# Performance work log

Measured on AMD Instinct MI355X. Metric: run time of the kernel, lower is better.

## Reference

```python
import jax, jax.numpy as jnp
import numpy as np

B, D = 8192, 2048
H1, H2, G = 1024, 512, 512
T, SPEC, SH = 2, 2, 2
E = T * SPEC + SH          # total experts = 6
EC = SPEC + SH             # experts per task = 4


def setup_inputs() -> dict:
    key = jax.random.key(0)
    ks = jax.random.split(key, 6)
    s = 0.02  # glorot-ish scale
    return {
        "x":   jax.random.normal(ks[0], (B, D), jnp.float32),
        "We1": jax.random.normal(ks[1], (E, D, H1), jnp.float32) * s,
        "be1": jnp.zeros((E, H1), jnp.float32),
        "We2": jax.random.normal(ks[2], (E, H1, H2), jnp.float32) * s,
        "be2": jnp.zeros((E, H2), jnp.float32),
        "Wg1": jax.random.normal(ks[3], (T, D, G), jnp.float32) * s,
        "bg1": jnp.zeros((T, G), jnp.float32),
        "Wgs": jax.random.normal(ks[4], (T, G, EC), jnp.float32) * s,
    }


# per-task expert indices: task i uses its SPEC specific experts + the SH shared (last) experts
_IDX = np.array([[i * SPEC + j for j in range(SPEC)] + list(range(T * SPEC, E))
                 for i in range(T)])  # [T, EC]


def reference(x, We1, be1, We2, be2, Wg1, bg1, Wgs):
    # All experts batched into grouped GEMMs (the fusion the original loop misses)
    h1 = jax.nn.relu(jnp.einsum('bd,edh->beh', x, We1) + be1)        # [B,E,H1]
    h2 = jax.nn.relu(jnp.einsum('beh,eho->beo', h1, We2) + be2)      # [B,E,H2]
    # Gate MLP per task, batched over tasks
    g = jax.nn.relu(jnp.einsum('bd,tdg->btg', x, Wg1) + bg1)         # [B,T,G]
    gate = jax.nn.softmax(jnp.einsum('btg,tge->bte', g, Wgs), axis=-1)  # [B,T,EC]
    sel = h2[:, _IDX, :]                                             # [B,T,EC,H2]
    out = jnp.einsum('bteo,bte->tbo', sel, gate)                     # [T,B,H2]
    return out
```

## Files before the change

kernel.cpp:

```cpp
#include <hip/hip_runtime.h>
#include <hip/hip_bf16.h>
#include <cstdint>
#include <cstddef>

#define B_   8192
#define D_   2048
#define H1_  1024
#define H2_  512
#define G_   512
#define T_   2
#define E_   6
#define EC_  4

typedef __bf16 bf16_t;
typedef __attribute__((ext_vector_type(8))) __bf16 bf16x8;
typedef __attribute__((ext_vector_type(4))) float f32x4;

__device__ __forceinline__ void gload_lds16(const bf16_t* g, bf16_t* l) {
    __builtin_amdgcn_global_load_lds(
        (const __attribute__((address_space(1))) bf16_t*)g,
        (__attribute__((address_space(3))) bf16_t*)l,
        16, 0, 0);
}

__global__ __launch_bounds__(256) void cast_x_kernel(
    const float* __restrict__ src, bf16_t* __restrict__ dst, int n8)
{
    int i = blockIdx.x * blockDim.x + threadIdx.x;
    if (i >= n8) return;
    const float4* s = (const float4*)src + (size_t)i * 2;
    float4 a = s[0], b = s[1];
    bf16x8 o;
    o[0] = (bf16_t)a.x; o[1] = (bf16_t)a.y; o[2] = (bf16_t)a.z; o[3] = (bf16_t)a.w;
    o[4] = (bf16_t)b.x; o[5] = (bf16_t)b.y; o[6] = (bf16_t)b.z; o[7] = (bf16_t)b.w;
    *(bf16x8*)(dst + (size_t)i * 8) = o;
}

__global__ __launch_bounds__(256) void transpose_cast_kernel(
    const float* __restrict__ src, bf16_t* __restrict__ dst, int R, int C)
{
    __shared__ float tile[32][33];
    int bz = blockIdx.z;
    src += (size_t)bz * R * C;
    dst += (size_t)bz * R * C;
    int c0 = blockIdx.x * 32, r0 = blockIdx.y * 32;
    int tx = threadIdx.x, ty = threadIdx.y;
#pragma unroll
    for (int i = 0; i < 32; i += 8)
        tile[ty + i][tx] = src[(size_t)(r0 + ty + i) * C + (c0 + tx)];
    __syncthreads();
#pragma unroll
    for (int i = 0; i < 32; i += 8)
        dst[(size_t)(c0 + ty + i) * R + (r0 + tx)] = (bf16_t)tile[tx][ty + i];
}

__global__ __launch_bounds__(512, 2) void gemm256_8p1b(
    const bf16_t* __restrict__ A, const bf16_t* __restrict__ Bt,
    const float* __restrict__ bias, bf16_t* __restrict__ C,
    int M, int N, int K, long long strideA)
{
    const int e = blockIdx.z;
    A    += (size_t)e * (size_t)strideA;
    Bt   += (size_t)e * (size_t)N * (size_t)K;
    bias += (size_t)e * (size_t)N;
    C    += (size_t)e * (size_t)M * (size_t)N;

    const int gx  = gridDim.x;
    const int nwg = gx * gridDim.y;
    const int lin = blockIdx.y * gx + blockIdx.x;
    const int swz = (lin & 7) * (nwg >> 3) + (lin >> 3);
    const int bx  = swz % gx;
    const int by  = swz / gx;
    const int row0 = by * 256;
    const int col0 = bx * 256;

    __shared__ bf16_t lsA[2][16384];
    __shared__ bf16_t lsB[2][16384];

    const int tid  = threadIdx.x;
    const int lane = tid & 63;
    const int wave = tid >> 6;
    const int wr   = wave >> 2;
    const int wc   = wave & 3;

    size_t offG[2];
    int    ldsOff[2];
#pragma unroll
    for (int l = 0; l < 2; ++l) {
        int idx = l * 512 + tid;
        int r   = idx >> 3;
        int c   = (idx & 7) ^ (r & 7);
        offG[l]   = (size_t)r * (size_t)K + (size_t)(c * 8);
        ldsOff[l] = l * 4096 + wave * 512;
    }
    const bf16_t* gA = A  + (size_t)row0 * (size_t)K;
    const bf16_t* gB = Bt + (size_t)col0 * (size_t)K;
    const size_t halfStride = (size_t)128 * (size_t)K;

    const int rbA = (wr * 128 + (lane & 15)) * 64;
    const int rbB = (wc * 64  + (lane & 15)) * 64;
    int xc[2];
#pragma unroll
    for (int ks = 0; ks < 2; ++ks)
        xc[ks] = (ks * 32 + ((lane >> 4) * 8)) ^ ((lane & 7) << 3);

    f32x4 acc[8][4];
#pragma unroll
    for (int m = 0; m < 8; ++m)
#pragma unroll
        for (int n = 0; n < 4; ++n)
            acc[m][n] = (f32x4){0.f, 0.f, 0.f, 0.f};

    const int nt    = K >> 6;
    const int niter = nt >> 1;

#define STAGE_A(dst, kt, h) do {                                              \
    _Pragma("unroll")                                                         \
    for (int l_ = 0; l_ < 2; ++l_)                                            \
        gload_lds16(gA + (size_t)((kt) * 64) + (size_t)(h) * halfStride       \
                       + offG[l_],                                            \
                    &lsA[dst][(h) * 8192 + ldsOff[l_]]);                      \
} while (0)

#define STAGE_B(dst, kt, h) do {                                              \
    _Pragma("unroll")                                                         \
    for (int l_ = 0; l_ < 2; ++l_)                                            \
        gload_lds16(gB + (size_t)((kt) * 64) + (size_t)(h) * halfStride       \
                       + offG[l_],                                            \
                    &lsB[dst][(h) * 8192 + ldsOff[l_]]);                      \
} while (0)

#define PHASE(d, qm, STMT, WAITV) do {                                        \
    bf16x8 af00, af01, af10, af11;                                            \
    af00 = *(const bf16x8*)&lsA[d][rbA + (2*(qm)+0) * 1024 + xc[0]];          \
    af01 = *(const bf16x8*)&lsA[d][rbA + (2*(qm)+0) * 1024 + xc[1]];          \
    af10 = *(const bf16x8*)&lsA[d][rbA + (2*(qm)+1) * 1024 + xc[0]];          \
    af11 = *(const bf16x8*)&lsA[d][rbA + (2*(qm)+1) * 1024 + xc[1]];          \
    if ((qm) == 0) {                                                          \
        _Pragma("unroll")                                                     \
        for (int n_ = 0; n_ < 4; ++n_) {                                      \
            bfr[n_][0] = *(const bf16x8*)&lsB[d][rbB + n_ * 1024 + xc[0]];    \
            bfr[n_][1] = *(const bf16x8*)&lsB[d][rbB + n_ * 1024 + xc[1]];    \
        }                                                                     \
    }                                                                         \
    STMT;                                                                     \
    WAITV;                                                                    \
    __builtin_amdgcn_sched_barrier(0);                                        \
    __builtin_amdgcn_s_barrier();                                             \
    asm volatile("s_waitcnt lgkmcnt(0)" ::: "memory");                        \
    __builtin_amdgcn_sched_barrier(0);                                        \
    __builtin_amdgcn_s_setprio(1);                                            \
    _Pragma("unroll")                                                         \
    for (int n_ = 0; n_ < 4; ++n_) {                                          \
        acc[2*(qm)+0][n_] = __builtin_amdgcn_mfma_f32_16x16x32_bf16(          \
                                af00, bfr[n_][0], acc[2*(qm)+0][n_], 0,0,0);  \
        acc[2*(qm)+0][n_] = __builtin_amdgcn_mfma_f32_16x16x32_bf16(          \
                                af01, bfr[n_][1], acc[2*(qm)+0][n_], 0,0,0);  \
        acc[2*(qm)+1][n_] = __builtin_amdgcn_mfma_f32_16x16x32_bf16(          \
                                af10, bfr[n_][0], acc[2*(qm)+1][n_], 0,0,0);  \
        acc[2*(qm)+1][n_] = __builtin_amdgcn_mfma_f32_16x16x32_bf16(          \
                                af11, bfr[n_][1], acc[2*(qm)+1][n_], 0,0,0);  \
    }                                                                         \
    __builtin_amdgcn_s_setprio(0);                                            \
    __builtin_amdgcn_sched_barrier(0);                                        \
} while (0)

    STAGE_A(0, 0, 0); STAGE_A(0, 0, 1);
    STAGE_B(0, 0, 0); STAGE_B(0, 0, 1);
    STAGE_B(1, 1, 0); STAGE_B(1, 1, 1);
    asm volatile("s_waitcnt vmcnt(4)" ::: "memory");
    __builtin_amdgcn_sched_barrier(0);
    __builtin_amdgcn_s_barrier();
    __builtin_amdgcn_sched_barrier(0);

    for (int i = 0; i < niter; ++i) {
        const int kt0 = 2 * i, kt1 = 2 * i + 1;
        const bool stg = (i + 1 < niter);
        bf16x8 bfr[4][2];

        PHASE(0, 0, { STAGE_A(1, kt1, 0); }, {});
        PHASE(0, 1, { STAGE_A(1, kt1, 1); }, {});
        PHASE(0, 2, { if (stg) STAGE_B(0, kt0 + 2, 0); }, {});
        PHASE(0, 3, { if (stg) STAGE_B(0, kt0 + 2, 1); },
              { if (stg) { asm volatile("s_waitcnt vmcnt(4)" ::: "memory"); }
                else     { asm volatile("s_waitcnt vmcnt(0)" ::: "memory"); } });
        PHASE(1, 0, { if (stg) STAGE_A(0, kt0 + 2, 0); }, {});
        PHASE(1, 1, { if (stg) STAGE_A(0, kt0 + 2, 1); }, {});
        PHASE(1, 2, { if (stg) STAGE_B(1, kt0 + 3, 0); }, {});
        PHASE(1, 3, { if (stg) STAGE_B(1, kt0 + 3, 1); },
              { if (stg) { asm volatile("s_waitcnt vmcnt(4)" ::: "memory"); } });
    }
#undef PHASE
#undef STAGE_A
#undef STAGE_B

    const int crb = row0 + wr * 128 + ((lane >> 4) << 2);
    const int ccb = col0 + wc * 64  + (lane & 15);
#pragma unroll
    for (int n = 0; n < 4; ++n) {
        const int cc = ccb + n * 16;
        const float bv = bias[cc];
#pragma unroll
        for (int m = 0; m < 8; ++m) {
            const int rb = crb + m * 16;
#pragma unroll
            for (int j = 0; j < 4; ++j) {
                float v = acc[m][n][j] + bv;
                v = v > 0.f ? v : 0.f;
                C[(size_t)(rb + j) * N + cc] = (bf16_t)v;
            }
        }
    }
}

__global__ __launch_bounds__(512, 4) void gemm_bn256_bias_relu(
    const bf16_t* __restrict__ A, const bf16_t* __restrict__ Bt,
    const float* __restrict__ bias, bf16_t* __restrict__ C,
    int M, int N, int K, long long strideA)
{
    const int e = blockIdx.z;
    A    += (size_t)e * (size_t)strideA;
    Bt   += (size_t)e * (size_t)N * (size_t)K;
    bias += (size_t)e * (size_t)N;
    C    += (size_t)e * (size_t)M * (size_t)N;

    const int gx  = gridDim.x;
    const int nwg = gx * gridDim.y;
    const int lin = blockIdx.y * gx + blockIdx.x;
    const int swz = (lin & 7) * (nwg >> 3) + (lin >> 3);
    const int row0 = (swz / gx) * 128;
    const int col0 = (swz % gx) * 256;

    __shared__ bf16_t lsA[3][128 * 32];
    __shared__ bf16_t lsB[3][256 * 32];

    const int tid  = threadIdx.x;
    const int lane = tid & 63;
    const int wave = tid >> 6;
    const int wr   = wave >> 2;
    const int wc   = wave & 3;

    size_t offA, offB0, offB1;
    {
        int rA = tid >> 2, pA = tid & 3;
        offA = (size_t)rA * (size_t)K + (size_t)(((pA ^ (rA >> 1)) & 3) * 8);
        int r0_ = tid >> 2, p0_ = tid & 3;
        offB0 = (size_t)r0_ * (size_t)K + (size_t)(((p0_ ^ (r0_ >> 1)) & 3) * 8);
        int r1_ = (512 + tid) >> 2, p1_ = tid & 3;
        offB1 = (size_t)r1_ * (size_t)K + (size_t)(((p1_ ^ (r1_ >> 1)) & 3) * 8);
    }
    const int ldsA_off = wave * 512;
    const int ldsB0off = wave * 512;
    const int ldsB1off = 4096 + wave * 512;

    const bf16_t* gA = A  + (size_t)row0 * (size_t)K;
    const bf16_t* gB = Bt + (size_t)col0 * (size_t)K;

    const int xch  = ((lane >> 4) ^ ((lane >> 1) & 3)) << 3;
    const int aoff = (wr * 64 + (lane & 15)) * 32 + xch;
    const int boff = (wc * 64 + (lane & 15)) * 32 + xch;

    f32x4 acc[4][4];
#pragma unroll
    for (int m = 0; m < 4; ++m)
#pragma unroll
        for (int n = 0; n < 4; ++n)
            acc[m][n] = (f32x4){0.f, 0.f, 0.f, 0.f};

    const int nt = K >> 5;

#define STAGE(t_, c_) do {                                                    \
    const size_t kk_ = (size_t)(t_) * 32;                                     \
    gload_lds16(gA + kk_ + offA,  &lsA[c_][ldsA_off]);                        \
    gload_lds16(gB + kk_ + offB0, &lsB[c_][ldsB0off]);                        \
    gload_lds16(gB + kk_ + offB1, &lsB[c_][ldsB1off]);                        \
} while (0)

    STAGE(0, 0); STAGE(1, 1); STAGE(2, 2);
    asm volatile("s_waitcnt vmcnt(6)" ::: "memory");
    __builtin_amdgcn_s_barrier();
    __builtin_amdgcn_sched_barrier(0);

    int c = 0;
    for (int t = 0; t < nt; ++t) {
        bf16x8 a[4], b[4];
#pragma unroll
        for (int m = 0; m < 4; ++m)
            a[m] = *(const bf16x8*)&lsA[c][aoff + m * 512];
#pragma unroll
        for (int n = 0; n < 4; ++n)
            b[n] = *(const bf16x8*)&lsB[c][boff + n * 512];
        asm volatile("s_waitcnt lgkmcnt(0)" ::: "memory");
        __builtin_amdgcn_sched_barrier(0);
        __builtin_amdgcn_s_barrier();
        __builtin_amdgcn_sched_barrier(0);
        if (t + 3 < nt) STAGE(t + 3, c);
        __builtin_amdgcn_sched_barrier(0);
        __builtin_amdgcn_s_setprio(1);
#pragma unroll
        for (int m = 0; m < 4; ++m)
#pragma unroll
            for (int n = 0; n < 4; ++n)
                acc[m][n] = __builtin_amdgcn_mfma_f32_16x16x32_bf16(
                                a[m], b[n], acc[m][n], 0, 0, 0);
        __builtin_amdgcn_s_setprio(0);
        __builtin_amdgcn_sched_barrier(0);
        if (t + 3 < nt) { asm volatile("s_waitcnt vmcnt(6)" ::: "memory"); }
        else            { asm volatile("s_waitcnt vmcnt(0)" ::: "memory"); }
        __builtin_amdgcn_sched_barrier(0);
        __builtin_amdgcn_s_barrier();
        __builtin_amdgcn_sched_barrier(0);
        c = (c == 2) ? 0 : c + 1;
    }
#undef STAGE

    const int crb = row0 + wr * 64 + ((lane >> 4) << 2);
    const int ccb = col0 + wc * 64 + (lane & 15);
#pragma unroll
    for (int n = 0; n < 4; ++n) {
        const int cc = ccb + n * 16;
        const float bv = bias[cc];
#pragma unroll
        for (int m = 0; m < 4; ++m) {
            const int rb = crb + m * 16;
#pragma unroll
            for (int j = 0; j < 4; ++j) {
                float v = acc[m][n][j] + bv;
                v = v > 0.f ? v : 0.f;
                C[(size_t)(rb + j) * N + cc] = (bf16_t)v;
            }
        }
    }
}

__global__ __launch_bounds__(256) void gate_kernel(
    const bf16_t* __restrict__ h1, const float* __restrict__ Wgs,
    float* __restrict__ gate)
{
    int wid  = blockIdx.x * 4 + (threadIdx.x >> 6);
    int lane = threadIdx.x & 63;
    int t = wid >> 13;
    int b = wid & (B_ - 1);
    const bf16_t* grow = h1 + ((size_t)(6 * B_) + b) * 1024 + t * G_;
    bf16x8 gv = *(const bf16x8*)&grow[lane * 8];
    const float* W = Wgs + (size_t)t * G_ * EC_;
    float a0 = 0.f, a1 = 0.f, a2 = 0.f, a3 = 0.f;
#pragma unroll
    for (int i = 0; i < 8; ++i) {
        float gvf = (float)gv[i];
        const float4 w = *(const float4*)&W[(size_t)(lane * 8 + i) * 4];
        a0 += gvf * w.x; a1 += gvf * w.y; a2 += gvf * w.z; a3 += gvf * w.w;
    }
#pragma unroll
    for (int off = 32; off; off >>= 1) {
        a0 += __shfl_xor(a0, off);
        a1 += __shfl_xor(a1, off);
        a2 += __shfl_xor(a2, off);
        a3 += __shfl_xor(a3, off);
    }
    if (lane == 0) {
        float m  = fmaxf(fmaxf(a0, a1), fmaxf(a2, a3));
        float e0 = expf(a0 - m), e1 = expf(a1 - m), e2 = expf(a2 - m), e3 = expf(a3 - m);
        float inv = 1.f / (e0 + e1 + e2 + e3);
        *(float4*)&gate[(size_t)wid * 4] = make_float4(e0 * inv, e1 * inv, e2 * inv, e3 * inv);
    }
}

__global__ __launch_bounds__(256) void combine_kernel(
    const bf16_t* __restrict__ h2, const float* __restrict__ gate,
    float* __restrict__ out)
{
    size_t idx = (size_t)blockIdx.x * 256 + threadIdx.x;
    size_t tb  = idx >> 6;
    int    o0  = (int)(idx & 63) * 8;
    int    t   = (int)(tb >> 13);
    size_t b   = tb & (size_t)(B_ - 1);
    const float4 gv = *(const float4*)&gate[tb * 4];
    const bf16x8 v0 = *(const bf16x8*)&h2[((size_t)(2 * t)     * B_ + b) * H2_ + o0];
    const bf16x8 v1 = *(const bf16x8*)&h2[((size_t)(2 * t + 1) * B_ + b) * H2_ + o0];
    const bf16x8 v2 = *(const bf16x8*)&h2[((size_t)4           * B_ + b) * H2_ + o0];
    const bf16x8 v3 = *(const bf16x8*)&h2[((size_t)5           * B_ + b) * H2_ + o0];
    float r[8];
#pragma unroll
    for (int i = 0; i < 8; ++i)
        r[i] = gv.x * (float)v0[i] + gv.y * (float)v1[i]
             + gv.z * (float)v2[i] + gv.w * (float)v3[i];
    float4* op = (float4*)&out[tb * H2_ + o0];
    op[0] = make_float4(r[0], r[1], r[2], r[3]);
    op[1] = make_float4(r[4], r[5], r[6], r[7]);
}

extern "C" void kernel_launch(void* const* d_in, const int* in_sizes, int n_in,
                              void* d_out, int out_size, void* d_ws, size_t ws_size,
                              hipStream_t stream)
{
    const float* x   = (const float*)d_in[0];
    const float* We1 = (const float*)d_in[1];
    const float* be1 = (const float*)d_in[2];
    const float* We2 = (const float*)d_in[3];
    const float* be2 = (const float*)d_in[4];
    const float* Wg1 = (const float*)d_in[5];
    const float* bg1 = (const float*)d_in[6];
    const float* Wgs = (const float*)d_in[7];
    float* out = (float*)d_out;

    char* ws = (char*)d_ws;
    bf16_t* x_bf  = (bf16_t*)ws;  ws += (size_t)B_ * D_ * 2;
    bf16_t* w1t   = (bf16_t*)ws;  ws += (size_t)7 * H1_ * D_ * 2;
    bf16_t* w2t   = (bf16_t*)ws;  ws += (size_t)E_ * H2_ * H1_ * 2;
    bf16_t* h1    = (bf16_t*)ws;  ws += (size_t)7 * B_ * H1_ * 2;
    bf16_t* h2    = (bf16_t*)ws;  ws += (size_t)E_ * B_ * H2_ * 2;
    float*  bias7 = (float*)ws;   ws += (size_t)7 * H1_ * 4;
    float*  gate  = (float*)ws;   ws += (size_t)T_ * B_ * EC_ * 4;

    bf16_t* wgt = w1t + (size_t)6 * H1_ * D_;

    hipMemcpyAsync(bias7, be1, (size_t)E_ * H1_ * sizeof(float),
                   hipMemcpyDeviceToDevice, stream);
    hipMemcpyAsync(bias7 + (size_t)E_ * H1_, bg1, (size_t)T_ * G_ * sizeof(float),
                   hipMemcpyDeviceToDevice, stream);

    cast_x_kernel<<<(B_ * D_ / 8) / 256, 256, 0, stream>>>(x, x_bf, B_ * D_ / 8);
    dim3 tb(32, 8);
    transpose_cast_kernel<<<dim3(H1_ / 32, D_ / 32, E_),  tb, 0, stream>>>(We1, w1t, D_,  H1_);
    transpose_cast_kernel<<<dim3(H2_ / 32, H1_ / 32, E_), tb, 0, stream>>>(We2, w2t, H1_, H2_);
    transpose_cast_kernel<<<dim3(G_ / 32, D_ / 32, T_),   tb, 0, stream>>>(Wg1, wgt, D_,  G_);

    gemm256_8p1b<<<dim3(H1_ / 256, B_ / 256, 7), 512, 0, stream>>>(
        x_bf, w1t, bias7, h1, B_, H1_, D_, 0LL);
    gemm_bn256_bias_relu<<<dim3(H2_ / 256, B_ / 128, E_), 512, 0, stream>>>(
        h1, w2t, be2, h2, B_, H2_, H1_, (long long)B_ * H1_);

    gate_kernel<<<(T_ * B_) / 4, 256, 0, stream>>>(h1, Wgs, gate);
    combine_kernel<<<((size_t)T_ * B_ * H2_ / 8) / 256, 256, 0, stream>>>(h2, gate, out);
}
```

Before: 383.8 us.

## Fuse gated combine into second GEMM epilogue with atomics; merge prep kernels

The second expert GEMM now scales its ReLU output by the per-row gate weights and atomically adds into the output. This removes the h2 intermediate buffer and the separate combine kernel, with the output zeroed by a memset beforehand. The x cast and the three weight transpose-casts are merged into one launch, and the first-layer bias now comes straight from be1/bg1, so the two device-to-device copies are gone. In exchange the epilogue issues scattered fp32 atomic adds (two per element for shared experts), and the summation order is no longer deterministic.

```diff
diff --git a/kernel.cpp b/kernel.cpp
--- a/kernel.cpp
+++ b/kernel.cpp
@@ -23,28 +23,42 @@
         16, 0, 0);
 }
 
-__global__ __launch_bounds__(256) void cast_x_kernel(
-    const float* __restrict__ src, bf16_t* __restrict__ dst, int n8)
-{
-    int i = blockIdx.x * blockDim.x + threadIdx.x;
-    if (i >= n8) return;
-    const float4* s = (const float4*)src + (size_t)i * 2;
-    float4 a = s[0], b = s[1];
-    bf16x8 o;
-    o[0] = (bf16_t)a.x; o[1] = (bf16_t)a.y; o[2] = (bf16_t)a.z; o[3] = (bf16_t)a.w;
-    o[4] = (bf16_t)b.x; o[5] = (bf16_t)b.y; o[6] = (bf16_t)b.z; o[7] = (bf16_t)b.w;
-    *(bf16x8*)(dst + (size_t)i * 8) = o;
-}
-
-__global__ __launch_bounds__(256) void transpose_cast_kernel(
-    const float* __restrict__ src, bf16_t* __restrict__ dst, int R, int C)
+__global__ __launch_bounds__(256) void prep_kernel(
+    const float* __restrict__ x,   const float* __restrict__ We1,
+    const float* __restrict__ We2, const float* __restrict__ Wg1,
+    bf16_t* __restrict__ x_bf, bf16_t* __restrict__ w1t,
+    bf16_t* __restrict__ w2t,  bf16_t* __restrict__ wgt)
 {
     __shared__ float tile[32][33];
-    int bz = blockIdx.z;
-    src += (size_t)bz * R * C;
-    dst += (size_t)bz * R * C;
-    int c0 = blockIdx.x * 32, r0 = blockIdx.y * 32;
-    int tx = threadIdx.x, ty = threadIdx.y;
+    const int z  = blockIdx.z;
+    const int bx = blockIdx.x, by = blockIdx.y;
+    const int tx = threadIdx.x, ty = threadIdx.y;
+
+    const float* src; bf16_t* dst; int R, C;
+    if (z < 6) {
+        src = We1 + (size_t)z * D_ * H1_;  dst = w1t + (size_t)z * H1_ * D_;
+        R = D_;  C = H1_;
+    } else if (z < 12) {
+        if (bx >= 16 || by >= 32) return;
+        src = We2 + (size_t)(z - 6) * H1_ * H2_;
+        dst = w2t + (size_t)(z - 6) * H2_ * H1_;
+        R = H1_; C = H2_;
+    } else if (z < 14) {
+        if (bx >= 16) return;
+        src = Wg1 + (size_t)(z - 12) * D_ * G_;
+        dst = wgt + (size_t)(z - 12) * G_ * D_;
+        R = D_;  C = G_;
+    } else {
+        int i = ((z - 14) * 2048 + by * 32 + bx) * 256 + ty * 32 + tx;
+        const float4* s = (const float4*)x + (size_t)i * 2;
+        float4 a = s[0], b = s[1];
+        bf16x8 o;
+        o[0] = (bf16_t)a.x; o[1] = (bf16_t)a.y; o[2] = (bf16_t)a.z; o[3] = (bf16_t)a.w;
+        o[4] = (bf16_t)b.x; o[5] = (bf16_t)b.y; o[6] = (bf16_t)b.z; o[7] = (bf16_t)b.w;
+        *(bf16x8*)(x_bf + (size_t)i * 8) = o;
+        return;
+    }
+    const int c0 = bx * 32, r0 = by * 32;
 #pragma unroll
     for (int i = 0; i < 32; i += 8)
         tile[ty + i][tx] = src[(size_t)(r0 + ty + i) * C + (c0 + tx)];
@@ -56,23 +70,21 @@
 
 __global__ __launch_bounds__(512, 2) void gemm256_8p1b(
     const bf16_t* __restrict__ A, const bf16_t* __restrict__ Bt,
-    const float* __restrict__ bias, bf16_t* __restrict__ C,
-    int M, int N, int K, long long strideA)
+    const float* __restrict__ be1, const float* __restrict__ bg1,
+    bf16_t* __restrict__ C, int M, int N, int K, long long strideA)
 {
     const int e = blockIdx.z;
-    A    += (size_t)e * (size_t)strideA;
-    Bt   += (size_t)e * (size_t)N * (size_t)K;
-    bias += (size_t)e * (size_t)N;
-    C    += (size_t)e * (size_t)M * (size_t)N;
+    A  += (size_t)e * (size_t)strideA;
+    Bt += (size_t)e * (size_t)N * (size_t)K;
+    C  += (size_t)e * (size_t)M * (size_t)N;
+    const float* bias = (e < 6) ? (be1 + (size_t)e * H1_) : bg1;
 
     const int gx  = gridDim.x;
     const int nwg = gx * gridDim.y;
     const int lin = blockIdx.y * gx + blockIdx.x;
     const int swz = (lin & 7) * (nwg >> 3) + (lin >> 3);
-    const int bx  = swz % gx;
-    const int by  = swz / gx;
-    const int row0 = by * 256;
-    const int col0 = bx * 256;
+    const int row0 = (swz / gx) * 256;
+    const int col0 = (swz % gx) * 256;
 
     __shared__ bf16_t lsA[2][16384];
     __shared__ bf16_t lsB[2][16384];
@@ -213,126 +225,6 @@
     }
 }
 
-__global__ __launch_bounds__(512, 4) void gemm_bn256_bias_relu(
-    const bf16_t* __restrict__ A, const bf16_t* __restrict__ Bt,
-    const float* __restrict__ bias, bf16_t* __restrict__ C,
-    int M, int N, int K, long long strideA)
-{
-    const int e = blockIdx.z;
-    A    += (size_t)e * (size_t)strideA;
-    Bt   += (size_t)e * (size_t)N * (size_t)K;
-    bias += (size_t)e * (size_t)N;
-    C    += (size_t)e * (size_t)M * (size_t)N;
-
-    const int gx  = gridDim.x;
-    const int nwg = gx * gridDim.y;
-    const int lin = blockIdx.y * gx + blockIdx.x;
-    const int swz = (lin & 7) * (nwg >> 3) + (lin >> 3);
-    const int row0 = (swz / gx) * 128;
-    const int col0 = (swz % gx) * 256;
-
-    __shared__ bf16_t lsA[3][128 * 32];
-    __shared__ bf16_t lsB[3][256 * 32];
-
-    const int tid  = threadIdx.x;
-    const int lane = tid & 63;
-    const int wave = tid >> 6;
-    const int wr   = wave >> 2;
-    const int wc   = wave & 3;
-
-    size_t offA, offB0, offB1;
-    {
-        int rA = tid >> 2, pA = tid & 3;
-        offA = (size_t)rA * (size_t)K + (size_t)(((pA ^ (rA >> 1)) & 3) * 8);
-        int r0_ = tid >> 2, p0_ = tid & 3;
-        offB0 = (size_t)r0_ * (size_t)K + (size_t)(((p0_ ^ (r0_ >> 1)) & 3) * 8);
-        int r1_ = (512 + tid) >> 2, p1_ = tid & 3;
-        offB1 = (size_t)r1_ * (size_t)K + (size_t)(((p1_ ^ (r1_ >> 1)) & 3) * 8);
-    }
-    const int ldsA_off = wave * 512;
-    const int ldsB0off = wave * 512;
-    const int ldsB1off = 4096 + wave * 512;
-
-    const bf16_t* gA = A  + (size_t)row0 * (size_t)K;
-    const bf16_t* gB = Bt + (size_t)col0 * (size_t)K;
-
-    const int xch  = ((lane >> 4) ^ ((lane >> 1) & 3)) << 3;
-    const int aoff = (wr * 64 + (lane & 15)) * 32 + xch;
-    const int boff = (wc * 64 + (lane & 15)) * 32 + xch;
-
-    f32x4 acc[4][4];
-#pragma unroll
-    for (int m = 0; m < 4; ++m)
-#pragma unroll
-        for (int n = 0; n < 4; ++n)
-            acc[m][n] = (f32x4){0.f, 0.f, 0.f, 0.f};
-
-    const int nt = K >> 5;
-
-#define STAGE(t_, c_) do {                                                    \
-    const size_t kk_ = (size_t)(t_) * 32;                                     \
-    gload_lds16(gA + kk_ + offA,  &lsA[c_][ldsA_off]);                        \
-    gload_lds16(gB + kk_ + offB0, &lsB[c_][ldsB0off]);                        \
-    gload_lds16(gB + kk_ + offB1, &lsB[c_][ldsB1off]);                        \
-} while (0)
-
-    STAGE(0, 0); STAGE(1, 1); STAGE(2, 2);
-    asm volatile("s_waitcnt vmcnt(6)" ::: "memory");
-    __builtin_amdgcn_s_barrier();
-    __builtin_amdgcn_sched_barrier(0);
-
-    int c = 0;
-    for (int t = 0; t < nt; ++t) {
-        bf16x8 a[4], b[4];
-#pragma unroll
-        for (int m = 0; m < 4; ++m)
-            a[m] = *(const bf16x8*)&lsA[c][aoff + m * 512];
-#pragma unroll
-        for (int n = 0; n < 4; ++n)
-            b[n] = *(const bf16x8*)&lsB[c][boff + n * 512];
-        asm volatile("s_waitcnt lgkmcnt(0)" ::: "memory");
-        __builtin_amdgcn_sched_barrier(0);
-        __builtin_amdgcn_s_barrier();
-        __builtin_amdgcn_sched_barrier(0);
-        if (t + 3 < nt) STAGE(t + 3, c);
-        __builtin_amdgcn_sched_barrier(0);
-        __builtin_amdgcn_s_setprio(1);
-#pragma unroll
-        for (int m = 0; m < 4; ++m)
-#pragma unroll
-            for (int n = 0; n < 4; ++n)
-                acc[m][n] = __builtin_amdgcn_mfma_f32_16x16x32_bf16(
-                                a[m], b[n], acc[m][n], 0, 0, 0);
-        __builtin_amdgcn_s_setprio(0);
-        __builtin_amdgcn_sched_barrier(0);
-        if (t + 3 < nt) { asm volatile("s_waitcnt vmcnt(6)" ::: "memory"); }
-        else            { asm volatile("s_waitcnt vmcnt(0)" ::: "memory"); }
-        __builtin_amdgcn_sched_barrier(0);
-        __builtin_amdgcn_s_barrier();
-        __builtin_amdgcn_sched_barrier(0);
-        c = (c == 2) ? 0 : c + 1;
-    }
-#undef STAGE
-
-    const int crb = row0 + wr * 64 + ((lane >> 4) << 2);
-    const int ccb = col0 + wc * 64 + (lane & 15);
-#pragma unroll
-    for (int n = 0; n < 4; ++n) {
-        const int cc = ccb + n * 16;
-        const float bv = bias[cc];
-#pragma unroll
-        for (int m = 0; m < 4; ++m) {
-            const int rb = crb + m * 16;
-#pragma unroll
-            for (int j = 0; j < 4; ++j) {
-                float v = acc[m][n][j] + bv;
-                v = v > 0.f ? v : 0.f;
-                C[(size_t)(rb + j) * N + cc] = (bf16_t)v;
-            }
-        }
-    }
-}
-
 __global__ __launch_bounds__(256) void gate_kernel(
     const bf16_t* __restrict__ h1, const float* __restrict__ Wgs,
     float* __restrict__ gate)
@@ -366,28 +258,138 @@
     }
 }
 
-__global__ __launch_bounds__(256) void combine_kernel(
-    const bf16_t* __restrict__ h2, const float* __restrict__ gate,
-    float* __restrict__ out)
+__global__ __launch_bounds__(512, 4) void gemm2_gated(
+    const bf16_t* __restrict__ A, const bf16_t* __restrict__ Bt,
+    const float* __restrict__ bias, const float* __restrict__ gate,
+    float* __restrict__ out, int M, int N, int K, long long strideA)
 {
-    size_t idx = (size_t)blockIdx.x * 256 + threadIdx.x;
-    size_t tb  = idx >> 6;
-    int    o0  = (int)(idx & 63) * 8;
-    int    t   = (int)(tb >> 13);
-    size_t b   = tb & (size_t)(B_ - 1);
-    const float4 gv = *(const float4*)&gate[tb * 4];
-    const bf16x8 v0 = *(const bf16x8*)&h2[((size_t)(2 * t)     * B_ + b) * H2_ + o0];
-    const bf16x8 v1 = *(const bf16x8*)&h2[((size_t)(2 * t + 1) * B_ + b) * H2_ + o0];
-    const bf16x8 v2 = *(const bf16x8*)&h2[((size_t)4           * B_ + b) * H2_ + o0];
-    const bf16x8 v3 = *(const bf16x8*)&h2[((size_t)5           * B_ + b) * H2_ + o0];
-    float r[8];
-#pragma unroll
-    for (int i = 0; i < 8; ++i)
-        r[i] = gv.x * (float)v0[i] + gv.y * (float)v1[i]
-             + gv.z * (float)v2[i] + gv.w * (float)v3[i];
-    float4* op = (float4*)&out[tb * H2_ + o0];
-    op[0] = make_float4(r[0], r[1], r[2], r[3]);
-    op[1] = make_float4(r[4], r[5], r[6], r[7]);
+    const int e = blockIdx.z;
+    A    += (size_t)e * (size_t)strideA;
+    Bt   += (size_t)e * (size_t)N * (size_t)K;
+    bias += (size_t)e * (size_t)N;
+
+    const int gx  = gridDim.x;
+    const int nwg = gx * gridDim.y;
+    const int lin = blockIdx.y * gx + blockIdx.x;
+    const int swz = (lin & 7) * (nwg >> 3) + (lin >> 3);
+    const int row0 = (swz / gx) * 128;
+    const int col0 = (swz % gx) * 256;
+
+    __shared__ bf16_t lsA[3][128 * 32];
+    __shared__ bf16_t lsB[3][256 * 32];
+
+    const int tid  = threadIdx.x;
+    const int lane = tid & 63;
+    const int wave = tid >> 6;
+    const int wr   = wave >> 2;
+    const int wc   = wave & 3;
+
+    size_t offA, offB0, offB1;
+    {
+        int rA = tid >> 2, pA = tid & 3;
+        offA = (size_t)rA * (size_t)K + (size_t)(((pA ^ (rA >> 1)) & 3) * 8);
+        int r0_ = tid >> 2, p0_ = tid & 3;
+        offB0 = (size_t)r0_ * (size_t)K + (size_t)(((p0_ ^ (r0_ >> 1)) & 3) * 8);
+        int r1_ = (512 + tid) >> 2, p1_ = tid & 3;
+        offB1 = (size_t)r1_ * (size_t)K + (size_t)(((p1_ ^ (r1_ >> 1)) & 3) * 8);
+    }
+    const int ldsA_off = wave * 512;
+    const int ldsB0off = wave * 512;
+    const int ldsB1off = 4096 + wave * 512;
+
+    const bf16_t* gA = A  + (size_t)row0 * (size_t)K;
+    const bf16_t* gB = Bt + (size_t)col0 * (size_t)K;
+
+    const int xch  = ((lane >> 4) ^ ((lane >> 1) & 3)) << 3;
+    const int aoff = (wr * 64 + (lane & 15)) * 32 + xch;
+    const int boff = (wc * 64 + (lane & 15)) * 32 + xch;
+
+    f32x4 acc[4][4];
+#pragma unroll
+    for (int m = 0; m < 4; ++m)
+#pragma unroll
+        for (int n = 0; n < 4; ++n)
+            acc[m][n] = (f32x4){0.f, 0.f, 0.f, 0.f};
+
+    const int nt = K >> 5;
+
+#define STAGE(t_, c_) do {                                                    \
+    const size_t kk_ = (size_t)(t_) * 32;                                     \
+    gload_lds16(gA + kk_ + offA,  &lsA[c_][ldsA_off]);                        \
+    gload_lds16(gB + kk_ + offB0, &lsB[c_][ldsB0off]);                        \
+    gload_lds16(gB + kk_ + offB1, &lsB[c_][ldsB1off]);                        \
+} while (0)
+
+    STAGE(0, 0); STAGE(1, 1); STAGE(2, 2);
+    asm volatile("s_waitcnt vmcnt(6)" ::: "memory");
+    __builtin_amdgcn_s_barrier();
+    __builtin_amdgcn_sched_barrier(0);
+
+    int c = 0;
+    for (int t = 0; t < nt; ++t) {
+        bf16x8 a[4], b[4];
+#pragma unroll
+        for (int m = 0; m < 4; ++m)
+            a[m] = *(const bf16x8*)&lsA[c][aoff + m * 512];
+#pragma unroll
+        for (int n = 0; n < 4; ++n)
+            b[n] = *(const bf16x8*)&lsB[c][boff + n * 512];
+        asm volatile("s_waitcnt lgkmcnt(0)" ::: "memory");
+        __builtin_amdgcn_sched_barrier(0);
+        __builtin_amdgcn_s_barrier();
+        __builtin_amdgcn_sched_barrier(0);
+        if (t + 3 < nt) STAGE(t + 3, c);
+        __builtin_amdgcn_sched_barrier(0);
+        __builtin_amdgcn_s_setprio(1);
+#pragma unroll
+        for (int m = 0; m < 4; ++m)
+#pragma unroll
+            for (int n = 0; n < 4; ++n)
+                acc[m][n] = __builtin_amdgcn_mfma_f32_16x16x32_bf16(
+                                a[m], b[n], acc[m][n], 0, 0, 0);
+        __builtin_amdgcn_s_setprio(0);
+        __builtin_amdgcn_sched_barrier(0);
+        if (t + 3 < nt) { asm volatile("s_waitcnt vmcnt(6)" ::: "memory"); }
+        else            { asm volatile("s_waitcnt vmcnt(0)" ::: "memory"); }
+        __builtin_amdgcn_sched_barrier(0);
+        __builtin_amdgcn_s_barrier();
+        __builtin_amdgcn_sched_barrier(0);
+        c = (c == 2) ? 0 : c + 1;
+    }
+#undef STAGE
+
+    int t0, j0, t1 = -1, j1 = 0;
+    switch (e) {
+        case 0:  t0 = 0; j0 = 0; break;
+        case 1:  t0 = 0; j0 = 1; break;
+        case 2:  t0 = 1; j0 = 0; break;
+        case 3:  t0 = 1; j0 = 1; break;
+        case 4:  t0 = 0; j0 = 2; t1 = 1; j1 = 2; break;
+        default: t0 = 0; j0 = 3; t1 = 1; j1 = 3; break;
+    }
+    const int crb = row0 + wr * 64 + ((lane >> 4) << 2);
+    const int ccb = col0 + wc * 64 + (lane & 15);
+#pragma unroll
+    for (int n = 0; n < 4; ++n) {
+        const int cc = ccb + n * 16;
+        const float bv = bias[cc];
+#pragma unroll
+        for (int m = 0; m < 4; ++m) {
+            const int rb = crb + m * 16;
+#pragma unroll
+            for (int j = 0; j < 4; ++j) {
+                const int b = rb + j;
+                float v = acc[m][n][j] + bv;
+                v = v > 0.f ? v : 0.f;
+                float g0 = gate[((size_t)t0 * B_ + b) * EC_ + j0];
+                unsafeAtomicAdd(&out[((size_t)t0 * B_ + b) * H2_ + cc], g0 * v);
+                if (t1 >= 0) {
+                    float g1 = gate[((size_t)t1 * B_ + b) * EC_ + j1];
+                    unsafeAtomicAdd(&out[((size_t)t1 * B_ + b) * H2_ + cc], g1 * v);
+                }
+            }
+        }
+    }
 }
 
 extern "C" void kernel_launch(void* const* d_in, const int* in_sizes, int n_in,
@@ -405,32 +407,24 @@
     float* out = (float*)d_out;
 
     char* ws = (char*)d_ws;
-    bf16_t* x_bf  = (bf16_t*)ws;  ws += (size_t)B_ * D_ * 2;
-    bf16_t* w1t   = (bf16_t*)ws;  ws += (size_t)7 * H1_ * D_ * 2;
-    bf16_t* w2t   = (bf16_t*)ws;  ws += (size_t)E_ * H2_ * H1_ * 2;
-    bf16_t* h1    = (bf16_t*)ws;  ws += (size_t)7 * B_ * H1_ * 2;
-    bf16_t* h2    = (bf16_t*)ws;  ws += (size_t)E_ * B_ * H2_ * 2;
-    float*  bias7 = (float*)ws;   ws += (size_t)7 * H1_ * 4;
-    float*  gate  = (float*)ws;   ws += (size_t)T_ * B_ * EC_ * 4;
+    bf16_t* x_bf = (bf16_t*)ws;  ws += (size_t)B_ * D_ * 2;
+    bf16_t* w1t  = (bf16_t*)ws;  ws += (size_t)7 * H1_ * D_ * 2;
+    bf16_t* w2t  = (bf16_t*)ws;  ws += (size_t)E_ * H2_ * H1_ * 2;
+    bf16_t* h1   = (bf16_t*)ws;  ws += (size_t)7 * B_ * H1_ * 2;
+    float*  gate = (float*)ws;   ws += (size_t)T_ * B_ * EC_ * 4;
 
     bf16_t* wgt = w1t + (size_t)6 * H1_ * D_;
 
-    hipMemcpyAsync(bias7, be1, (size_t)E_ * H1_ * sizeof(float),
-                   hipMemcpyDeviceToDevice, stream);
-    hipMemcpyAsync(bias7 + (size_t)E_ * H1_, bg1, (size_t)T_ * G_ * sizeof(float),
-                   hipMemcpyDeviceToDevice, stream);
-
-    cast_x_kernel<<<(B_ * D_ / 8) / 256, 256, 0, stream>>>(x, x_bf, B_ * D_ / 8);
-    dim3 tb(32, 8);
-    transpose_cast_kernel<<<dim3(H1_ / 32, D_ / 32, E_),  tb, 0, stream>>>(We1, w1t, D_,  H1_);
-    transpose_cast_kernel<<<dim3(H2_ / 32, H1_ / 32, E_), tb, 0, stream>>>(We2, w2t, H1_, H2_);
-    transpose_cast_kernel<<<dim3(G_ / 32, D_ / 32, T_),   tb, 0, stream>>>(Wg1, wgt, D_,  G_);
+    hipMemsetAsync(out, 0, (size_t)T_ * B_ * H2_ * sizeof(float), stream);
+
+    prep_kernel<<<dim3(32, 64, 18), dim3(32, 8), 0, stream>>>(
+        x, We1, We2, Wg1, x_bf, w1t, w2t, wgt);
 
     gemm256_8p1b<<<dim3(H1_ / 256, B_ / 256, 7), 512, 0, stream>>>(
-        x_bf, w1t, bias7, h1, B_, H1_, D_, 0LL);
-    gemm_bn256_bias_relu<<<dim3(H2_ / 256, B_ / 128, E_), 512, 0, stream>>>(
-        h1, w2t, be2, h2, B_, H2_, H1_, (long long)B_ * H1_);
+        x_bf, w1t, be1, bg1, h1, B_, H1_, D_, 0LL);
 
     gate_kernel<<<(T_ * B_) / 4, 256, 0, stream>>>(h1, Wgs, gate);
-    combine_kernel<<<((size_t)T_ * B_ * H2_ / 8) / 256, 256, 0, stream>>>(h2, gate, out);
-}
+
+    gemm2_gated<<<dim3(H2_ / 256, B_ / 128, E_), 512, 0, stream>>>(
+        h1, w2t, be2, gate, out, B_, H2_, H1_, (long long)B_ * H1_);
+}
```

Measured after the change: 436.9 us. 13.8% more time.
